# Kernel tuning notes

Measured on AMD Instinct MI355X. Metric: run time of the kernel, lower is better.

The kernel has to match this reference:

```python
import jax, jax.numpy as jnp
import numpy as np
from jax import lax

STRIDE = 16
SCALE = 16.0
ANCHOR_DIMS = (1.0, 2.0, 4.0, 8.0, 16.0, 32.0)
PRE_NMS_TOP_N = 6000
POST_NMS_TOP_N = 300
NMS_THRESH = 0.7


def conv2d(x, w, b, pad):
    y = lax.conv_general_dilated(x, w, (1, 1), [(pad, pad), (pad, pad)],
                                 dimension_numbers=("NCHW", "OIHW", "NCHW"))
    return y + b[None, :, None, None]


def setup_inputs() -> dict:
    key = jax.random.key(0)
    ks = jax.random.split(key, 6)
    B, C, H, W = 1, 1024, 128, 128
    A = len(ANCHOR_DIMS)
    return {
        "base_features": jax.random.normal(ks[0], (B, C, H, W), jnp.float32),
        "image_metadata": jnp.array([[H * STRIDE, W * STRIDE, 1.0]], jnp.float32),
        "gt_boxes": jax.random.uniform(ks[1], (B, 20, 5), jnp.float32) * 100.0,
        "W_conv": jax.random.normal(ks[2], (512, C, 3, 3), jnp.float32) / np.sqrt(C * 9.0),
        "b_conv": jnp.zeros((512,), jnp.float32),
        "W_cls": jax.random.normal(ks[3], (A, 512, 1, 1), jnp.float32) / np.sqrt(512.0),
        "b_cls": jnp.zeros((A,), jnp.float32),
        "W_bbox": jax.random.normal(ks[4], (4 * A, 512, 1, 1), jnp.float32) * 0.01,
        "b_bbox": jnp.zeros((4 * A,), jnp.float32),
    }


def _make_anchors(H, W):
    # square anchors of size dim*scale, centered on each feature cell
    dims = jnp.asarray(ANCHOR_DIMS, jnp.float32) * SCALE          # [A]
    cy = (jnp.arange(H, dtype=jnp.float32) + 0.5) * STRIDE        # [H]
    cx = (jnp.arange(W, dtype=jnp.float32) + 0.5) * STRIDE        # [W]
    half = 0.5 * dims[None, None, :]                              # [1,1,A]
    CX = cx[None, :, None]
    CY = cy[:, None, None]
    anchors = jnp.stack(jnp.broadcast_arrays(CX - half, CY - half, CX + half, CY + half), axis=-1)
    return anchors.reshape(-1, 4)                                 # [(H*W*A),4], order (h,w,a)


def _nms_fixed(boxes, scores):
    # boxes [N,4] already sorted by score desc; greedy NMS, POST_NMS_TOP_N picks
    x1, y1, x2, y2 = boxes[:, 0], boxes[:, 1], boxes[:, 2], boxes[:, 3]
    areas = jnp.maximum(x2 - x1, 0.0) * jnp.maximum(y2 - y1, 0.0)

    def body(i, state):
        alive, keep = state
        masked = jnp.where(alive, scores, -jnp.inf)
        j = jnp.argmax(masked)
        valid = masked[j] > -jnp.inf
        keep = keep.at[i].set(jnp.where(valid, j, -1).astype(jnp.int32))
        bj = boxes[j]
        iw = jnp.maximum(jnp.minimum(x2, bj[2]) - jnp.maximum(x1, bj[0]), 0.0)
        ih = jnp.maximum(jnp.minimum(y2, bj[3]) - jnp.maximum(y1, bj[1]), 0.0)
        inter = iw * ih
        iou = inter / (areas + areas[j] - inter + 1e-9)
        alive = alive & (iou <= NMS_THRESH)
        return alive, keep

    alive0 = jnp.ones(boxes.shape[0], bool)
    keep0 = jnp.full((POST_NMS_TOP_N,), -1, jnp.int32)
    _, keep = lax.fori_loop(0, POST_NMS_TOP_N, body, (alive0, keep0))
    return keep


def _proposal(prob, bbox, image_metadata):
    # original layer operates on detached tensors (.data)
    prob = lax.stop_gradient(prob)
    bbox = lax.stop_gradient(bbox)
    B, A, H, W = prob.shape
    anchors = _make_anchors(H, W)                                 # [N,4]
    scores = prob[0].transpose(1, 2, 0).reshape(-1)               # (h,w,a)
    deltas = bbox[0].reshape(A, 4, H, W).transpose(2, 3, 0, 1).reshape(-1, 4)
    wa = anchors[:, 2] - anchors[:, 0]
    ha = anchors[:, 3] - anchors[:, 1]
    cxa = anchors[:, 0] + 0.5 * wa
    cya = anchors[:, 1] + 0.5 * ha
    pcx = deltas[:, 0] * wa + cxa
    pcy = deltas[:, 1] * ha + cya
    pw = jnp.exp(deltas[:, 2]) * wa
    ph = jnp.exp(deltas[:, 3]) * ha
    boxes = jnp.stack([pcx - 0.5 * pw, pcy - 0.5 * ph, pcx + 0.5 * pw, pcy + 0.5 * ph], axis=1)
    im_h, im_w = image_metadata[0, 0], image_metadata[0, 1]
    boxes = jnp.stack([
        jnp.clip(boxes[:, 0], 0.0, im_w), jnp.clip(boxes[:, 1], 0.0, im_h),
        jnp.clip(boxes[:, 2], 0.0, im_w), jnp.clip(boxes[:, 3], 0.0, im_h)], axis=1)
    top_scores, top_idx = lax.top_k(scores, PRE_NMS_TOP_N)
    top_boxes = boxes[top_idx]
    keep = _nms_fixed(top_boxes, top_scores)
    sel = jnp.where(keep >= 0, keep, 0)
    kept = top_boxes[sel] * (keep >= 0).astype(top_boxes.dtype)[:, None]
    rois = jnp.concatenate([jnp.zeros((POST_NMS_TOP_N, 1), top_boxes.dtype), kept], axis=1)
    return rois                                                   # [POST_NMS_TOP_N, 5]


def reference(base_features, image_metadata, gt_boxes, W_conv, b_conv, W_cls, b_cls, W_bbox, b_bbox):
    conv1 = jax.nn.relu(conv2d(base_features, W_conv, b_conv, pad=1))   # [B,512,H,W]
    score = conv2d(conv1, W_cls, b_cls, pad=0)                          # [B,A,H,W]
    B, A, H, W = score.shape
    s2 = score.reshape(B, 2, (A * H) // 2, W)                           # RPN.reshape(x, 2)
    prob = jax.nn.softmax(s2, axis=1).reshape(B, A, H, W)               # reshape back to A channels
    bbox = conv2d(conv1, W_bbox, b_bbox, pad=0)                         # [B,4A,H,W]
    rois = _proposal(prob, bbox, image_metadata)
    return rois, prob, bbox
```

## Files before the change

### kernel.cpp

```cpp
#include <hip/hip_runtime.h>
#include <math.h>

typedef unsigned int u32;
typedef unsigned long long u64;
typedef short s16x8 __attribute__((ext_vector_type(8)));
typedef float f32x4 __attribute__((ext_vector_type(4)));

#define HH 128
#define WW 128
#define NPIX (128*128)
#define NANCH (NPIX*6)
#define KPRE 6000
#define KPOST 300
#define SORT_CAP 16384
#define RW 96
#define NMS_T 0.7f

#define OUT_PROB 1500
#define OUT_BBOX (1500 + 98304)

#define WS_CONV1 ((size_t)0)
#define WS_XTH   ((size_t)33554432)
#define WS_WPH   ((size_t)100663296)
#define WS_BOXES ((size_t)33554432)
#define WS_SCORE (WS_BOXES + 1572864)
#define WS_KEYS  (WS_SCORE + 393216)
#define WS_TB    (WS_KEYS + 131072)
#define WS_AREA  (WS_TB + 98304)
#define WS_SUP   (WS_AREA + 24576)
#define WS_HIST  (WS_SUP + 4718592)
#define WS_CTRL  (WS_HIST + 262144)
#define WS_KEEP  (WS_CTRL + 256)
#define WS_SKEYS (WS_KEEP + 1280)

__device__ __forceinline__ unsigned short f2bf(float x) {
    u32 b = __float_as_uint(x);
    u32 r = (b + 0x7FFFu + ((b >> 16) & 1u)) >> 16;
    return (unsigned short)r;
}

__device__ __forceinline__ void gl_lds16(const void* g, void* l) {
    __builtin_amdgcn_global_load_lds(
        (__attribute__((address_space(1))) const void*)g,
        (__attribute__((address_space(3))) void*)l,
        16, 0, 0);
}

__global__ void k_init(u32* __restrict__ hist, u32* __restrict__ ctrl,
                       int* __restrict__ keep, u64* __restrict__ keys) {
    int t = blockIdx.x * blockDim.x + threadIdx.x;
    if (t < 65536) hist[t] = 0u;
    if (t < 64)    ctrl[t] = 0u;
    if (t < 304)   keep[t] = -1;
    if (t < SORT_CAP) keys[t] = ~0ULL;
}

__global__ __launch_bounds__(256) void k_xsplit(const float* __restrict__ in,
                                                unsigned short* __restrict__ xth) {
    unsigned short* xtl = xth + 16777216;
    __shared__ unsigned short Th[64][72];
    __shared__ unsigned short Tl[64][72];
    const int px0 = blockIdx.x * 64;
    const int c0  = blockIdx.y * 64;
    const int t = threadIdx.x;
    const int r = t >> 4;
    const int p4 = (t & 15) * 4;
#pragma unroll
    for (int i = 0; i < 4; ++i) {
        int cr = r + 16 * i;
        float4 v = *(const float4*)(in + (size_t)(c0 + cr) * NPIX + px0 + p4);
        float vv[4] = {v.x, v.y, v.z, v.w};
#pragma unroll
        for (int k = 0; k < 4; ++k) {
            unsigned short h = f2bf(vv[k]);
            float hf = __uint_as_float((u32)h << 16);
            unsigned short l = f2bf(vv[k] - hf);
            Th[p4 + k][cr] = h;
            Tl[p4 + k][cr] = l;
        }
    }
    __syncthreads();
    const int p = t >> 2, q = t & 3;
    unsigned short* dh = xth + (size_t)(px0 + p) * 1024 + c0 + q * 16;
    unsigned short* dl = xtl + (size_t)(px0 + p) * 1024 + c0 + q * 16;
    *(uint4*)dh       = *(const uint4*)&Th[p][q * 16];
    *(uint4*)(dh + 8) = *(const uint4*)&Th[p][q * 16 + 8];
    *(uint4*)dl       = *(const uint4*)&Tl[p][q * 16];
    *(uint4*)(dl + 8) = *(const uint4*)&Tl[p][q * 16 + 8];
}

__global__ __launch_bounds__(256) void k_wpack(const float* __restrict__ w,
                                               unsigned short* __restrict__ wph,
                                               float* __restrict__ zstash) {
    if (blockIdx.x == 0 && threadIdx.x < 128) zstash[threadIdx.x] = 0.f;
    int id = blockIdx.x * 256 + threadIdx.x;
    int oc = id >> 10, c = id & 1023;
    const float* src = w + (size_t)oc * 9216 + c * 9;
#pragma unroll
    for (int tap = 0; tap < 9; ++tap) {
        float x = src[tap];
        unsigned short h = f2bf(x);
        unsigned short l = f2bf(x - __uint_as_float((u32)h << 16));
        wph[(size_t)tap * 524288 + id] = h;
        wph[4718592 + (size_t)tap * 524288 + id] = l;
    }
}

__global__ __launch_bounds__(256, 2) void k_conv3m(const unsigned short* __restrict__ xt,
                                                   const unsigned short* __restrict__ wp,
                                                   const float* __restrict__ bias,
                                                   const unsigned short* __restrict__ zst,
                                                   float* __restrict__ out) {
    const int ocg = blockIdx.x;
    const int y   = blockIdx.y;
    const int oc0 = ocg * 128;
    const int tid = threadIdx.x;
    const int lane = tid & 63;
    const int w    = tid >> 6;
    const int l15  = lane & 15;
    const int quad = lane >> 4;
    const int hoc  = w >> 1, hpx = w & 1;

    __shared__ __align__(16) unsigned short Lds[32768];

    const int lg  = lane & 3;
    const int lr  = lane >> 2;

    const unsigned short* xsrc[4];
    int xstep[4];
    const unsigned short* wsrc[4];

    int wp_pl[4], wp_ocr[4], wp_gs[4];
#pragma unroll
    for (int j = 0; j < 4; ++j) {
        int i = w + 4 * j;
        wp_pl[j]  = i >> 3;
        wp_ocr[j] = (i & 7) * 16 + lr;
        wp_gs[j]  = lg ^ ((wp_ocr[j] >> 1) & 3);
    }
    int xp_pl[4], xp_p[4], xp_gs[4];
#pragma unroll
    for (int j = 0; j < 4; ++j) {
        int i = w + 4 * j;
        xp_pl[j] = i >> 3;
        xp_p[j]  = (i & 7) * 16 + lr;
        xp_gs[j] = lg ^ ((xp_p[j] >> 1) & 3);
    }

    auto set_tap = [&](int tap) {
        int dy = tap / 3, dx = tap - dy * 3;
        int yy = y + dy - 1;
        bool yok = (yy >= 0) && (yy < HH);
#pragma unroll
        for (int j = 0; j < 4; ++j) {
            int x = dx - 1 + xp_p[j];
            bool ok = yok && (x >= 0) && (x < WW);
            xsrc[j] = ok ? xt + (size_t)xp_pl[j] * 16777216
                              + (size_t)(yy * WW + x) * 1024 + xp_gs[j] * 8
                         : zst + lg * 8;
            xstep[j] = ok ? 32 : 0;
        }
#pragma unroll
        for (int j = 0; j < 4; ++j)
            wsrc[j] = wp + (size_t)wp_pl[j] * 4718592 + (size_t)tap * 524288
                        + (size_t)(oc0 + wp_ocr[j]) * 1024 + wp_gs[j] * 8;
    };

    auto issue = [&](int sel) {
        const int bo = sel * 16384;
#pragma unroll
        for (int j = 0; j < 4; ++j) {
            gl_lds16(xsrc[j], &Lds[bo + (w + 4 * j) * 512]);
            xsrc[j] += xstep[j];
        }
#pragma unroll
        for (int j = 0; j < 4; ++j) {
            gl_lds16(wsrc[j], &Lds[bo + 8192 + (w + 4 * j) * 512]);
            wsrc[j] += 32;
        }
    };

    const int g  = quad ^ ((l15 >> 1) & 3);
    const int bB0 = (hpx * 64 + l15) * 32 + g * 8;
    const int bA0 = 8192 + (hoc * 64 + l15) * 32 + g * 8;

    f32x4 acc[4][4];
#pragma unroll
    for (int og = 0; og < 4; ++og)
#pragma unroll
        for (int nt = 0; nt < 4; ++nt) acc[og][nt] = (f32x4){0.f, 0.f, 0.f, 0.f};

    set_tap(0);
    issue(0);

    for (int s = 0; s < 288; ++s) {
        const int cur = s & 1;
        __syncthreads();
        if (s + 1 < 288) {
            int s1 = s + 1;
            if ((s1 & 31) == 0) set_tap(s1 >> 5);
            issue(s1 & 1);
        }

        const int bo = cur * 16384;
        s16x8 ah[4], al[4];
#pragma unroll
        for (int og = 0; og < 4; ++og) {
            ah[og] = *(const s16x8*)&Lds[bo + bA0 + og * 512];
            al[og] = *(const s16x8*)&Lds[bo + bA0 + 4096 + og * 512];
        }
#pragma unroll
        for (int nt = 0; nt < 4; ++nt) {
            const s16x8 bh = *(const s16x8*)&Lds[bo + bB0 + nt * 512];
            const s16x8 bl = *(const s16x8*)&Lds[bo + bB0 + 4096 + nt * 512];
#pragma unroll
            for (int og = 0; og < 4; ++og) {
                acc[og][nt] = __builtin_amdgcn_mfma_f32_16x16x32_bf16(ah[og], bh, acc[og][nt], 0, 0, 0);
                acc[og][nt] = __builtin_amdgcn_mfma_f32_16x16x32_bf16(ah[og], bl, acc[og][nt], 0, 0, 0);
                acc[og][nt] = __builtin_amdgcn_mfma_f32_16x16x32_bf16(al[og], bh, acc[og][nt], 0, 0, 0);
            }
        }
    }

#pragma unroll
    for (int og = 0; og < 4; ++og) {
#pragma unroll
        for (int nt = 0; nt < 4; ++nt) {
#pragma unroll
            for (int rg = 0; rg < 4; ++rg) {
                const int oc = oc0 + hoc * 64 + og * 16 + quad * 4 + rg;
                const int px = hpx * 64 + nt * 16 + l15;
                float v = acc[og][nt][rg] + bias[oc];
                out[(size_t)oc * NPIX + y * WW + px] = fmaxf(v, 0.f);
            }
        }
    }
}

__global__ __launch_bounds__(256) void k_conv1(const float* __restrict__ conv1,
                                               const float* __restrict__ wcls,
                                               const float* __restrict__ bcls,
                                               const float* __restrict__ wbox,
                                               const float* __restrict__ bboxb,
                                               float* __restrict__ out) {
    const int tid = threadIdx.x;
    const int og = tid >> 4, pg = tid & 15;
    const int px0 = blockIdx.x * 64;
    __shared__ __align__(16) float Wl[32][32];
    __shared__ __align__(16) float Xl[32][64];
    __shared__ float Sc[6][64];

    float a0[4] = {0, 0, 0, 0}, a1[4] = {0, 0, 0, 0};

    for (int cc = 0; cc < 16; ++cc) {
        {
            int u = tid;
            int row = (u * 4) >> 5;
            int col = (u * 4) & 31;
            float4 v;
            if (row < 6)       v = *(const float4*)(wcls + row * 512 + cc * 32 + col);
            else if (row < 30) v = *(const float4*)(wbox + (row - 6) * 512 + cc * 32 + col);
            else               v = make_float4(0.f, 0.f, 0.f, 0.f);
            *(float4*)&Wl[row][col] = v;
        }
        for (int u = tid; u < 512; u += 256) {
            int row = (u * 4) >> 6, col = (u * 4) & 63;
            *(float4*)&Xl[row][col] =
                *(const float4*)(conv1 + (size_t)(cc * 32 + row) * NPIX + px0 + col);
        }
        __syncthreads();
#pragma unroll
        for (int cp = 0; cp < 32; ++cp) {
            const float4 x = *(const float4*)&Xl[cp][pg * 4];
            const float w0 = Wl[og][cp];
            const float w1 = Wl[og + 16][cp];
            a0[0] = fmaf(w0, x.x, a0[0]); a0[1] = fmaf(w0, x.y, a0[1]);
            a0[2] = fmaf(w0, x.z, a0[2]); a0[3] = fmaf(w0, x.w, a0[3]);
            a1[0] = fmaf(w1, x.x, a1[0]); a1[1] = fmaf(w1, x.y, a1[1]);
            a1[2] = fmaf(w1, x.z, a1[2]); a1[3] = fmaf(w1, x.w, a1[3]);
        }
        __syncthreads();
    }
    const int pxb = px0 + pg * 4;
    if (og < 6) {
        const float bc = bcls[og];
#pragma unroll
        for (int kk = 0; kk < 4; ++kk) Sc[og][pg * 4 + kk] = a0[kk] + bc;
    } else {
        const float bb = bboxb[og - 6];
#pragma unroll
        for (int kk = 0; kk < 4; ++kk)
            out[OUT_BBOX + (size_t)(og - 6) * NPIX + pxb + kk] = a0[kk] + bb;
    }
    if (og + 16 < 30) {
        const float bb = bboxb[og + 10];
#pragma unroll
        for (int kk = 0; kk < 4; ++kk)
            out[OUT_BBOX + (size_t)(og + 10) * NPIX + pxb + kk] = a1[kk] + bb;
    }
    __syncthreads();
    if (og < 6) {
        const int pa = og < 3 ? og + 3 : og - 3;
#pragma unroll
        for (int kk = 0; kk < 4; ++kk) {
            const float s = Sc[og][pg * 4 + kk], sp = Sc[pa][pg * 4 + kk];
            out[OUT_PROB + (size_t)og * NPIX + pxb + kk] = 1.0f / (1.0f + expf(sp - s));
        }
    }
}

__global__ void k_decode(const float* __restrict__ out, const float* __restrict__ meta,
                         float4* __restrict__ boxes, float* __restrict__ scores) {
#pragma clang fp contract(off)
    int t = blockIdx.x * blockDim.x + threadIdx.x;
    if (t >= NANCH) return;
    int a = t >> 14;
    int pix = t & 16383;
    int yc = pix >> 7, xc = pix & 127;
    int n = pix * 6 + a;
    float sc = out[OUT_PROB + (size_t)a * NPIX + pix];
    float d0 = out[OUT_BBOX + (size_t)(a * 4 + 0) * NPIX + pix];
    float d1 = out[OUT_BBOX + (size_t)(a * 4 + 1) * NPIX + pix];
    float d2 = out[OUT_BBOX + (size_t)(a * 4 + 2) * NPIX + pix];
    float d3 = out[OUT_BBOX + (size_t)(a * 4 + 3) * NPIX + pix];
    const float dims = (float)(16 << a);
    const float cxa = (xc + 0.5f) * 16.f;
    const float cya = (yc + 0.5f) * 16.f;
    float pcx = d0 * dims + cxa;
    float pcy = d1 * dims + cya;
    float pw  = expf(d2) * dims;
    float ph  = expf(d3) * dims;
    float imh = meta[0], imw = meta[1];
    float x1 = fminf(fmaxf(pcx - 0.5f * pw, 0.f), imw);
    float y1 = fminf(fmaxf(pcy - 0.5f * ph, 0.f), imh);
    float x2 = fminf(fmaxf(pcx + 0.5f * pw, 0.f), imw);
    float y2 = fminf(fmaxf(pcy + 0.5f * ph, 0.f), imh);
    boxes[n] = make_float4(x1, y1, x2, y2);
    scores[n] = sc;
}

__global__ void k_hist(const float* __restrict__ scores, u32* __restrict__ hist) {
    int t = blockIdx.x * blockDim.x + threadIdx.x;
    if (t >= NANCH) return;
    u32 b = __float_as_uint(scores[t]) >> 16;
    atomicAdd(&hist[b], 1u);
}

__global__ void k_select(const u32* __restrict__ hist, u32* __restrict__ ctrl) {
    __shared__ u32 S[256];
    __shared__ u32 U[256];
    const int tid = threadIdx.x;
    u32 s = 0;
    for (int i = 0; i < 256; ++i) s += hist[tid * 256 + i];
    S[tid] = s;
    __syncthreads();
    if (tid == 0) {
        u32 acc = 0;
        for (int t2 = 255; t2 >= 0; --t2) { U[t2] = acc; acc += S[t2]; }
    }
    __syncthreads();
    if (U[tid] < KPRE && U[tid] + S[tid] >= KPRE) {
        u32 acc = U[tid];
        for (int b = tid * 256 + 255; b >= tid * 256; --b) {
            u32 h = hist[b];
            if (acc + h >= KPRE) { ctrl[1] = (u32)b; ctrl[2] = acc; break; }
            acc += h;
        }
    }
}

__global__ void k_compact(const float* __restrict__ scores, u32* __restrict__ ctrl,
                          u64* __restrict__ keys) {
    int t = blockIdx.x * blockDim.x + threadIdx.x;
    if (t >= NANCH) return;
    u32 bits = __float_as_uint(scores[t]);
    if ((bits >> 16) >= ctrl[1]) {
        u32 pos = atomicAdd(&ctrl[0], 1u);
        if (pos < SORT_CAP) keys[pos] = ((u64)(~bits) << 32) | (u32)t;
    }
}

__global__ __launch_bounds__(1024) void k_sort_local(u64* __restrict__ keys) {
    __shared__ u64 lds[8192];
    const int tid = threadIdx.x;
    u64* g = keys + blockIdx.x * 8192;
    for (int u = tid; u < 8192; u += 1024) lds[u] = g[u];
    __syncthreads();
    for (int k = 2; k <= 8192; k <<= 1) {
        for (int j = k >> 1; j > 0; j >>= 1) {
            for (int u = tid; u < 4096; u += 1024) {
                int i = ((u & ~(j - 1)) << 1) | (u & (j - 1));
                int l = i | j;
                bool up = (i & k) == 0;
                u64 x = lds[i], y2 = lds[l];
                if ((x > y2) == up) { lds[i] = y2; lds[l] = x; }
            }
            __syncthreads();
        }
    }
    for (int u = tid; u < 8192; u += 1024) g[u] = lds[u];
}

__global__ void k_merge(const u64* __restrict__ keys, u64* __restrict__ skeys) {
    int i = blockIdx.x * blockDim.x + threadIdx.x;
    if (i >= KPRE) return;
    const u64* A = keys;
    const u64* B = keys + 8192;
    int lo = i > 8192 ? i - 8192 : 0;
    int hi = i < 8192 ? i : 8192;
    while (lo < hi) {
        int a = (lo + hi) >> 1;
        if (A[a] < B[i - a - 1]) lo = a + 1; else hi = a;
    }
    int a = lo, b = i - lo;
    u64 va = (a < 8192) ? A[a] : ~0ULL;
    u64 vb = (b < 8192) ? B[b] : ~0ULL;
    skeys[i] = va < vb ? va : vb;
}

__global__ void k_gather(const u64* __restrict__ skeys, const float4* __restrict__ boxes,
                         float4* __restrict__ tb, float* __restrict__ areas) {
#pragma clang fp contract(off)
    int i = blockIdx.x * blockDim.x + threadIdx.x;
    if (i >= KPRE) return;
    u32 n = (u32)(skeys[i] & 0xFFFFFFFFULL);
    float4 b = boxes[n];
    tb[i] = b;
    areas[i] = fmaxf(b.z - b.x, 0.f) * fmaxf(b.w - b.y, 0.f);
}

__global__ __launch_bounds__(256) void k_bitmap(const float4* __restrict__ tb,
                                                const float* __restrict__ areas,
                                                u64* __restrict__ suppr) {
#pragma clang fp contract(off)
    const int i = blockIdx.x;
    const int lane = threadIdx.x & 63;
    const int wv = threadIdx.x >> 6;
    const float4 bi = tb[i];
    const float ai = areas[i];
    for (int Wd = wv; Wd < RW; Wd += 4) {
        int j = Wd * 64 + lane;
        bool sup = false;
        if (j < KPRE) {
            float4 bj = tb[j];
            float iw = fmaxf(fminf(bi.z, bj.z) - fmaxf(bi.x, bj.x), 0.f);
            float ih = fmaxf(fminf(bi.w, bj.w) - fmaxf(bi.y, bj.y), 0.f);
            float inter = iw * ih;
            float denom = ((areas[j] + ai) - inter) + 1e-9f;
            sup = (inter / denom) > NMS_T;
        }
        u64 m = __ballot(sup);
        if (lane == 0) suppr[(size_t)i * RW + Wd] = m;
    }
}

__global__ void k_scan(const u64* __restrict__ suppr, int* __restrict__ keep) {
    const int lane = threadIdx.x;
    u64 a0 = (lane < 93) ? ~0ULL : (lane == 93 ? ((1ULL << 48) - 1) : 0ULL);
    const int w1 = lane + 64;
    u64 a1 = (w1 < 93) ? ~0ULL : (w1 == 93 ? ((1ULL << 48) - 1) : 0ULL);
    int kept = 0;
    int i = 0;
    while (kept < KPOST) {
        int wi = i >> 6;
        if (wi >= 94) break;
        u64 wvv = (wi < 64) ? __shfl(a0, wi) : __shfl(a1, wi - 64);
        wvv &= (~0ULL) << (i & 63);
        if (wvv == 0ULL) { i = (wi + 1) << 6; continue; }
        int b = __ffsll((long long)wvv) - 1;
        i = (wi << 6) + b;
        if (lane == 0) keep[kept] = i;
        kept++;
        const u64* row = suppr + (size_t)i * RW;
        u64 s0 = row[lane];
        u64 s1 = (lane + 64 < RW) ? row[lane + 64] : 0ULL;
        a0 &= ~s0;
        a1 &= ~s1;
        i++;
    }
}

__global__ void k_rois(const int* __restrict__ keep, const float4* __restrict__ tb,
                       float* __restrict__ out) {
    int r = blockIdx.x * blockDim.x + threadIdx.x;
    if (r >= KPOST) return;
    int k = keep[r];
    float4 b = make_float4(0.f, 0.f, 0.f, 0.f);
    if (k >= 0) b = tb[k];
    out[r * 5 + 0] = 0.f;
    out[r * 5 + 1] = b.x;
    out[r * 5 + 2] = b.y;
    out[r * 5 + 3] = b.z;
    out[r * 5 + 4] = b.w;
}

extern "C" void kernel_launch(void* const* d_in, const int* in_sizes, int n_in,
                              void* d_out, int out_size, void* d_ws, size_t ws_size,
                              hipStream_t stream) {
    (void)in_sizes; (void)n_in; (void)out_size; (void)ws_size;
    const float* x     = (const float*)d_in[0];
    const float* meta  = (const float*)d_in[1];
    const float* wc3   = (const float*)d_in[3];
    const float* bc3   = (const float*)d_in[4];
    const float* wcls  = (const float*)d_in[5];
    const float* bcls  = (const float*)d_in[6];
    const float* wbox  = (const float*)d_in[7];
    const float* bboxb = (const float*)d_in[8];
    float* out = (float*)d_out;
    char* ws = (char*)d_ws;

    float*  conv1  = (float*)(ws + WS_CONV1);
    float4* boxes  = (float4*)(ws + WS_BOXES);
    float*  scores = (float*)(ws + WS_SCORE);
    u64*    keys   = (u64*)(ws + WS_KEYS);
    float4* tb     = (float4*)(ws + WS_TB);
    float*  areas  = (float*)(ws + WS_AREA);
    u64*    suppr  = (u64*)(ws + WS_SUP);
    u32*    hist   = (u32*)(ws + WS_HIST);
    u32*    ctrl   = (u32*)(ws + WS_CTRL);
    int*    keep   = (int*)(ws + WS_KEEP);
    u64*    skeys  = (u64*)(ws + WS_SKEYS);

    float* zstash = out;

    unsigned short* xth = (unsigned short*)(ws + WS_XTH);
    unsigned short* wph = (unsigned short*)(ws + WS_WPH);
    k_xsplit<<<dim3(256, 16), 256, 0, stream>>>(x, xth);
    k_wpack<<<2048, 256, 0, stream>>>(wc3, wph, zstash);
    k_conv3m<<<dim3(4, 128), 256, 0, stream>>>(xth, wph, bc3,
                                               (const unsigned short*)zstash, conv1);

    k_init<<<256, 256, 0, stream>>>(hist, ctrl, keep, keys);
    k_conv1<<<256, 256, 0, stream>>>(conv1, wcls, bcls, wbox, bboxb, out);
    k_decode<<<384, 256, 0, stream>>>(out, meta, boxes, scores);
    k_hist<<<384, 256, 0, stream>>>(scores, hist);
    k_select<<<1, 256, 0, stream>>>(hist, ctrl);
    k_compact<<<384, 256, 0, stream>>>(scores, ctrl, keys);
    k_sort_local<<<2, 1024, 0, stream>>>(keys);
    k_merge<<<24, 256, 0, stream>>>(keys, skeys);
    k_gather<<<24, 256, 0, stream>>>(skeys, boxes, tb, areas);
    k_bitmap<<<6000, 256, 0, stream>>>(tb, areas, suppr);
    k_scan<<<1, 64, 0, stream>>>(suppr, keep);
    k_rois<<<2, 256, 0, stream>>>(keep, tb, out);
}
```

Measured before the change: 936.8 us.

## Remap conv blocks per XCD, fuse hist/decode and merge/gather, skip lower bitmap

Flattens the 3x3 conv grid and remaps block ids so each XCD processes a contiguous band of rows across all output-channel groups, aiming at better L2 reuse of overlapping input rows. Fuses the score histogram atomics into the decode kernel and merges the merge-path and gather kernels, removing launches and intermediate buffers. The NMS bitmap kernel skips 64-bit words entirely below the diagonal, leaving them unwritten; this relies on the scan only reading words at or above each row's own word.

```diff
diff --git a/kernel.cpp b/kernel.cpp
--- a/kernel.cpp
+++ b/kernel.cpp
@@ -31,7 +31,6 @@
 #define WS_HIST  (WS_SUP + 4718592)
 #define WS_CTRL  (WS_HIST + 262144)
 #define WS_KEEP  (WS_CTRL + 256)
-#define WS_SKEYS (WS_KEEP + 1280)
 
 __device__ __forceinline__ unsigned short f2bf(float x) {
     u32 b = __float_as_uint(x);
@@ -111,8 +110,11 @@
                                                    const float* __restrict__ bias,
                                                    const unsigned short* __restrict__ zst,
                                                    float* __restrict__ out) {
-    const int ocg = blockIdx.x;
-    const int y   = blockIdx.y;
+    const int bid = blockIdx.x;
+    const int xcd = bid & 7;
+    const int kk  = bid >> 3;
+    const int ocg = kk & 3;
+    const int y   = xcd * 16 + (kk >> 2);
     const int oc0 = ocg * 128;
     const int tid = threadIdx.x;
     const int lane = tid & 63;
@@ -310,7 +312,8 @@
 }
 
 __global__ void k_decode(const float* __restrict__ out, const float* __restrict__ meta,
-                         float4* __restrict__ boxes, float* __restrict__ scores) {
+                         float4* __restrict__ boxes, float* __restrict__ scores,
+                         u32* __restrict__ hist) {
 #pragma clang fp contract(off)
     int t = blockIdx.x * blockDim.x + threadIdx.x;
     if (t >= NANCH) return;
@@ -337,13 +340,7 @@
     float y2 = fminf(fmaxf(pcy + 0.5f * ph, 0.f), imh);
     boxes[n] = make_float4(x1, y1, x2, y2);
     scores[n] = sc;
-}
-
-__global__ void k_hist(const float* __restrict__ scores, u32* __restrict__ hist) {
-    int t = blockIdx.x * blockDim.x + threadIdx.x;
-    if (t >= NANCH) return;
-    u32 b = __float_as_uint(scores[t]) >> 16;
-    atomicAdd(&hist[b], 1u);
+    atomicAdd(&hist[__float_as_uint(sc) >> 16], 1u);
 }
 
 __global__ void k_select(const u32* __restrict__ hist, u32* __restrict__ ctrl) {
@@ -401,7 +398,10 @@
     for (int u = tid; u < 8192; u += 1024) g[u] = lds[u];
 }
 
-__global__ void k_merge(const u64* __restrict__ keys, u64* __restrict__ skeys) {
+__global__ void k_mergegather(const u64* __restrict__ keys,
+                              const float4* __restrict__ boxes,
+                              float4* __restrict__ tb, float* __restrict__ areas) {
+#pragma clang fp contract(off)
     int i = blockIdx.x * blockDim.x + threadIdx.x;
     if (i >= KPRE) return;
     const u64* A = keys;
@@ -415,18 +415,11 @@
     int a = lo, b = i - lo;
     u64 va = (a < 8192) ? A[a] : ~0ULL;
     u64 vb = (b < 8192) ? B[b] : ~0ULL;
-    skeys[i] = va < vb ? va : vb;
-}
-
-__global__ void k_gather(const u64* __restrict__ skeys, const float4* __restrict__ boxes,
-                         float4* __restrict__ tb, float* __restrict__ areas) {
-#pragma clang fp contract(off)
-    int i = blockIdx.x * blockDim.x + threadIdx.x;
-    if (i >= KPRE) return;
-    u32 n = (u32)(skeys[i] & 0xFFFFFFFFULL);
-    float4 b = boxes[n];
-    tb[i] = b;
-    areas[i] = fmaxf(b.z - b.x, 0.f) * fmaxf(b.w - b.y, 0.f);
+    u64 v = va < vb ? va : vb;
+    u32 n = (u32)(v & 0xFFFFFFFFULL);
+    float4 bx = boxes[n];
+    tb[i] = bx;
+    areas[i] = fmaxf(bx.z - bx.x, 0.f) * fmaxf(bx.w - bx.y, 0.f);
 }
 
 __global__ __launch_bounds__(256) void k_bitmap(const float4* __restrict__ tb,
@@ -438,7 +431,8 @@
     const int wv = threadIdx.x >> 6;
     const float4 bi = tb[i];
     const float ai = areas[i];
-    for (int Wd = wv; Wd < RW; Wd += 4) {
+    const int w0 = i >> 6;
+    for (int Wd = w0 + wv; Wd < RW; Wd += 4) {
         int j = Wd * 64 + lane;
         bool sup = false;
         if (j < KPRE) {
@@ -519,7 +513,6 @@
     u32*    hist   = (u32*)(ws + WS_HIST);
     u32*    ctrl   = (u32*)(ws + WS_CTRL);
     int*    keep   = (int*)(ws + WS_KEEP);
-    u64*    skeys  = (u64*)(ws + WS_SKEYS);
 
     float* zstash = out;
 
@@ -527,18 +520,16 @@
     unsigned short* wph = (unsigned short*)(ws + WS_WPH);
     k_xsplit<<<dim3(256, 16), 256, 0, stream>>>(x, xth);
     k_wpack<<<2048, 256, 0, stream>>>(wc3, wph, zstash);
-    k_conv3m<<<dim3(4, 128), 256, 0, stream>>>(xth, wph, bc3,
-                                               (const unsigned short*)zstash, conv1);
+    k_conv3m<<<512, 256, 0, stream>>>(xth, wph, bc3,
+                                      (const unsigned short*)zstash, conv1);
 
     k_init<<<256, 256, 0, stream>>>(hist, ctrl, keep, keys);
     k_conv1<<<256, 256, 0, stream>>>(conv1, wcls, bcls, wbox, bboxb, out);
-    k_decode<<<384, 256, 0, stream>>>(out, meta, boxes, scores);
-    k_hist<<<384, 256, 0, stream>>>(scores, hist);
+    k_decode<<<384, 256, 0, stream>>>(out, meta, boxes, scores, hist);
     k_select<<<1, 256, 0, stream>>>(hist, ctrl);
     k_compact<<<384, 256, 0, stream>>>(scores, ctrl, keys);
     k_sort_local<<<2, 1024, 0, stream>>>(keys);
-    k_merge<<<24, 256, 0, stream>>>(keys, skeys);
-    k_gather<<<24, 256, 0, stream>>>(skeys, boxes, tb, areas);
+    k_mergegather<<<24, 256, 0, stream>>>(keys, boxes, tb, areas);
     k_bitmap<<<6000, 256, 0, stream>>>(tb, areas, suppr);
     k_scan<<<1, 64, 0, stream>>>(suppr, keep);
     k_rois<<<2, 256, 0, stream>>>(keep, tb, out);
```

Result: faster. 891.6 us (-4.8%).
